# Kernel tuning notes

Measured on AMD Instinct MI355X. Metric: run time of the kernel, lower is better.

Reference implementation:

```python
import jax, jax.numpy as jnp
import numpy as np

NUM_EMBEDDINGS = 2048
BATCH_SIZE = 8
SEQ_LEN = 512
SPATIAL_DIM = 1024
EMBED_DIM = BATCH_SIZE * SEQ_LEN  # 4096
COMMITMENT_COST = 0.25


def setup_inputs() -> dict:
    key = jax.random.key(0)
    k1, k2 = jax.random.split(key)
    inputs = jax.random.normal(k1, (BATCH_SIZE, SEQ_LEN, SPATIAL_DIM), dtype=jnp.float32)
    # original init: uniform(-1/K, 1/K); scaled normal is an acceptable stand-in scale
    embedding = jax.random.uniform(k2, (NUM_EMBEDDINGS, EMBED_DIM), dtype=jnp.float32,
                                   minval=-1.0 / NUM_EMBEDDINGS, maxval=1.0 / NUM_EMBEDDINGS)
    return {"inputs": inputs, "embedding": embedding}


def reference(inputs, embedding):
    B, L, S = inputs.shape
    K, D = embedding.shape
    sg = jax.lax.stop_gradient
    # [S, D] : one feature vector per spatial feature index
    x = jnp.transpose(inputs, (2, 0, 1)).reshape(S, -1)
    # squared-euclidean distances via expansion (avoids S x K x D intermediate)
    d = (jnp.sum(x * x, axis=1, keepdims=True)
         - 2.0 * jnp.einsum('sd,kd->sk', x, embedding)
         + jnp.sum(embedding * embedding, axis=1)[None, :])  # [S, K]
    idx = jnp.argmin(d, axis=1)                 # [S]
    q = embedding[idx]                          # [S, D] gather == one_hot @ E
    # per-feature losses (mse over the (1, D) feature vector == mean over D)
    e_latent = jnp.mean((sg(q) - x) ** 2, axis=1)
    q_latent = jnp.mean((q - sg(x)) ** 2, axis=1)
    total_loss = jnp.mean(q_latent + COMMITMENT_COST * e_latent)
    # straight-through estimator
    q_ste = x + sg(q - x)
    quantized_output = jnp.transpose(q_ste.reshape(S, B, L), (1, 2, 0))  # [B, L, S]
    # per-feature perplexity: encodings is (1, K) one-hot, avg over dim0 is the row itself
    enc = jax.nn.one_hot(idx, K, dtype=x.dtype)  # [S, K]
    perpl = jnp.exp(-jnp.sum(enc * jnp.log(enc + 1e-10), axis=1))  # [S]
    avg_perplexity = jnp.mean(perpl)
    return (total_loss, quantized_output, avg_perplexity, idx)
```

## Files before the change

kernel.cpp:

```cpp
#include <hip/hip_runtime.h>
#include <hip/hip_bf16.h>
#include <math.h>

#define S_DIM 1024
#define K_DIM 2048
#define D_DIM 4096

#define OUT_Q    1
#define OUT_PERP (1 + D_DIM * S_DIM)
#define OUT_IDX  (2 + D_DIM * S_DIM)

#define MARGIN 6.0e-3f
#define CONF_GAP 4.5e-3f
#define FLT_BIG 3.4028235e38f

#define WS_LOSS   0
#define WS_XX     64
#define WS_EE     4160
#define WS_MINP   77888
#define WS_CNT    143424
#define WS_IDX    208960
#define WS_KCAND  213056
#define WS_SCAND  2310208
#define WS_ESTAGE 4407360
#define WS_XSTAGE 21184576
#define WS_BEST   29573184
#define WS_PAIRS  29581376
#define WS_EEP    30105664ull
#define WS_XXP2   31154240ull
#define WS_NEEDED3 31678528ull

#define FB_LOSS 0
#define FB_XX   4096
#define FB_EE   8192
#define FB_XXP  16384
#define FB_MINV 81920
#define FB_MINI 212992
#define FB_IDX  344064

typedef __attribute__((ext_vector_type(8))) short bf16x8;
typedef __attribute__((ext_vector_type(4))) float f32x4;

__device__ __forceinline__ unsigned short f2bf(float f) {
    __hip_bfloat16 h = __float2bfloat16(f);
    return *reinterpret_cast<unsigned short*>(&h);
}

__device__ __forceinline__ void gload16(const void* g, void* l) {
    __builtin_amdgcn_global_load_lds(
        (const __attribute__((address_space(1))) unsigned int*)(g),
        (__attribute__((address_space(3))) unsigned int*)(l), 16, 0, 0);
}

__global__ __launch_bounds__(256) void k_xx_part(const float* __restrict__ A, float* __restrict__ xxp) {
    const int dc = blockIdx.x;
    const int s = blockIdx.y * 256 + threadIdx.x;
    float acc = 0.f;
    for (int dd = 0; dd < 256; ++dd) {
        const int d = dc * 256 + dd;
        float v = A[(size_t)d * S_DIM + s];
        acc = fmaf(v, v, acc);
    }
    xxp[dc * S_DIM + s] = acc;
}

__global__ __launch_bounds__(256) void k_xx_comb(const float* __restrict__ xxp, float* __restrict__ xx) {
    const int s = blockIdx.x * 256 + threadIdx.x;
    float acc = 0.f;
    for (int dc = 0; dc < 16; ++dc) acc += xxp[dc * S_DIM + s];
    xx[s] = acc;
}

__global__ __launch_bounds__(256) void k_ee(const float* __restrict__ E, float* __restrict__ ee) {
    const int k = blockIdx.x;
    const float4* row = (const float4*)(E + (size_t)k * D_DIM);
    float acc = 0.f;
#pragma unroll
    for (int j = 0; j < 4; ++j) {
        float4 v = row[threadIdx.x + j * 256];
        acc = fmaf(v.x, v.x, acc);
        acc = fmaf(v.y, v.y, acc);
        acc = fmaf(v.z, v.z, acc);
        acc = fmaf(v.w, v.w, acc);
    }
    __shared__ float red[256];
    red[threadIdx.x] = acc;
    __syncthreads();
    for (int off = 128; off > 0; off >>= 1) {
        if (threadIdx.x < off) red[threadIdx.x] += red[threadIdx.x + off];
        __syncthreads();
    }
    if (threadIdx.x == 0) ee[k] = red[0];
}

__global__ __launch_bounds__(256) void k_conv(const float* __restrict__ E, const float* __restrict__ A,
                                              float* __restrict__ AT, char* __restrict__ Estage,
                                              char* __restrict__ Xstage, float* __restrict__ eep,
                                              float* __restrict__ xxp2) {
    __shared__ float ldsT[32][65];
    const int dt = blockIdx.x;
    const int tid = threadIdx.x;
    if (blockIdx.y < 16) {
        const int kt = blockIdx.y;
        char* tile = Estage + (size_t)kt * 1048576 + (size_t)dt * 8192;
#pragma unroll
        for (int i = 0; i < 2; ++i) {
            int idx = i * 256 + tid;
            int row = idx >> 2, dc = idx & 3;
            const float4* src = (const float4*)(E + (size_t)(kt * 128 + row) * D_DIM + dt * 32 + dc * 8);
            float4 v0 = src[0], v1 = src[1];
            float vals[8] = {v0.x, v0.y, v0.z, v0.w, v1.x, v1.y, v1.z, v1.w};
            unsigned int w[4];
#pragma unroll
            for (int q = 0; q < 4; ++q)
                w[q] = (unsigned int)f2bf(vals[2 * q]) | ((unsigned int)f2bf(vals[2 * q + 1]) << 16);
            int c_dst = ((row >> 6) * 4 + ((row >> 4) & 3)) * 64 + dc * 16 + (row & 15);
            *(uint4*)(tile + (size_t)c_dst * 16) = make_uint4(w[0], w[1], w[2], w[3]);
            float p = 0.f;
#pragma unroll
            for (int q = 0; q < 8; ++q) p = fmaf(vals[q], vals[q], p);
            p += __shfl_down(p, 2);
            p += __shfl_down(p, 1);
            if ((tid & 3) == 0) eep[(size_t)dt * K_DIM + kt * 128 + row] = p;
        }
    } else {
        const int st = blockIdx.y - 16;
#pragma unroll
        for (int i = 0; i < 2; ++i) {
            int idx = i * 256 + tid;
            int row_d = idx >> 4, c = idx & 15;
            float4 v = *(const float4*)(A + (size_t)(dt * 32 + row_d) * S_DIM + st * 64 + c * 4);
            ldsT[row_d][c * 4 + 0] = v.x;
            ldsT[row_d][c * 4 + 1] = v.y;
            ldsT[row_d][c * 4 + 2] = v.z;
            ldsT[row_d][c * 4 + 3] = v.w;
        }
        __syncthreads();
        {
            int s_row = tid >> 2, dpart = (tid & 3) * 8;
            float vals[8];
#pragma unroll
            for (int j = 0; j < 8; ++j) vals[j] = ldsT[dpart + j][s_row];
            float* dst = AT + (size_t)(st * 64 + s_row) * D_DIM + dt * 32 + dpart;
            *(float4*)(dst + 0) = make_float4(vals[0], vals[1], vals[2], vals[3]);
            *(float4*)(dst + 4) = make_float4(vals[4], vals[5], vals[6], vals[7]);
            float p = 0.f;
#pragma unroll
            for (int j = 0; j < 8; ++j) p = fmaf(vals[j], vals[j], p);
            p += __shfl_down(p, 2);
            p += __shfl_down(p, 1);
            if ((tid & 3) == 0) xxp2[(size_t)dt * S_DIM + st * 64 + s_row] = p;
        }
        {
            int s_row = tid >> 2, dc = tid & 3;
            float vals[8];
#pragma unroll
            for (int j = 0; j < 8; ++j) vals[j] = ldsT[dc * 8 + j][s_row];
            unsigned int w[4];
#pragma unroll
            for (int q = 0; q < 4; ++q)
                w[q] = (unsigned int)f2bf(vals[2 * q]) | ((unsigned int)f2bf(vals[2 * q + 1]) << 16);
            int gn = ((s_row >> 5) << 1) | ((s_row >> 4) & 1);
            int c_dst = gn * 64 + dc * 16 + (s_row & 15);
            char* tile = Xstage + (size_t)st * 524288 + (size_t)dt * 4096;
            *(uint4*)(tile + (size_t)c_dst * 16) = make_uint4(w[0], w[1], w[2], w[3]);
        }
    }
}

__global__ __launch_bounds__(256) void k_sums(const float* __restrict__ eep, const float* __restrict__ xxp2,
                                              float* __restrict__ ee, float* __restrict__ xx,
                                              unsigned long long* __restrict__ best) {
    const int gid = blockIdx.x * 256 + threadIdx.x;
    if (gid < 1024) best[gid] = 0xFFFFFFFFFFFFFFFFull;
    if (gid < K_DIM) {
        float a = 0.f;
        for (int dt = 0; dt < 128; ++dt) a += eep[(size_t)dt * K_DIM + gid];
        ee[gid] = a;
    } else if (gid < K_DIM + S_DIM) {
        const int s = gid - K_DIM;
        float a = 0.f;
        for (int dt = 0; dt < 128; ++dt) a += xxp2[(size_t)dt * S_DIM + s];
        xx[s] = a;
    }
}

__global__ __launch_bounds__(1024) void k_gemm_score5(const char* __restrict__ Estage, const char* __restrict__ Xstage,
                                                      const float* __restrict__ xx, const float* __restrict__ ee,
                                                      float* __restrict__ minp, int* __restrict__ cnt,
                                                      int* __restrict__ kcand, float* __restrict__ scand) {
    __shared__ short lds[4 * 3 * 6144];
    __shared__ float minw[2][64];
    __shared__ float minb[64];
    __shared__ int cntl[64];

    const int linear = blockIdx.y * 16 + blockIdx.x;
    const int xcd = linear & 7, ii = linear >> 3;
    const int ktb = (xcd >> 1) * 4 + (ii >> 3);
    const int st  = (xcd & 1) * 8 + (ii & 7);

    const int tid = threadIdx.x;
    const int h = tid >> 8;
    const int tidh = tid & 255;
    const int wid2 = tidh >> 6;
    const int wm = wid2 >> 1;
    const int wn = wid2 & 1;
    const int lane = tid & 63;
    const int lr = lane & 15;
    const int lh = lane >> 4;

    const char* Eb = Estage + (size_t)ktb * 1048576;
    const char* Xb = Xstage + (size_t)st * 524288;
    short* myl = lds + h * 18432;

    f32x4 acc[4][2];
#pragma unroll
    for (int f = 0; f < 4; ++f)
#pragma unroll
        for (int g = 0; g < 2; ++g) acc[f][g] = (f32x4){0.f, 0.f, 0.f, 0.f};

#define STG(t, sl) { \
    const char* eb_ = Eb + (size_t)(h * 32 + (t)) * 8192; \
    char* d_ = (char*)myl + (sl) * 12288; \
    gload16(eb_ + tidh * 16, d_ + tidh * 16); \
    gload16(eb_ + 4096 + tidh * 16, d_ + 4096 + tidh * 16); \
    gload16(Xb + (size_t)(h * 32 + (t)) * 4096 + tidh * 16, d_ + 8192 + tidh * 16); }

#define CMP(sl) { \
    const short* s_ = myl + (sl) * 6144; \
    bf16x8 af[4], bx[2]; \
    _Pragma("unroll") \
    for (int f = 0; f < 4; ++f) af[f] = *(const bf16x8*)(s_ + (wm * 4 + f) * 512 + lane * 8); \
    _Pragma("unroll") \
    for (int g = 0; g < 2; ++g) bx[g] = *(const bf16x8*)(s_ + 4096 + (wn * 2 + g) * 512 + lane * 8); \
    _Pragma("unroll") \
    for (int f = 0; f < 4; ++f) { \
        _Pragma("unroll") \
        for (int g = 0; g < 2; ++g) \
            acc[f][g] = __builtin_amdgcn_mfma_f32_16x16x32_bf16(af[f], bx[g], acc[f][g], 0, 0, 0); \
    } }

#define WB(nstr) asm volatile("s_waitcnt vmcnt(" nstr ")\n\ts_barrier" ::: "memory")
#define BAR asm volatile("s_barrier" ::: "memory")

    STG(0, 0) STG(1, 1)

    for (int bb = 0; bb < 30; bb += 3) {
        STG(bb + 2, 2) WB("6"); CMP(0) BAR;
        STG(bb + 3, 0) WB("6"); CMP(1) BAR;
        STG(bb + 4, 1) WB("6"); CMP(2) BAR;
    }
    WB("3"); CMP(0) BAR;
    WB("0"); CMP(1)
    __syncthreads();

#undef STG
#undef CMP
#undef WB
#undef BAR

    f32x4* red4 = (f32x4*)lds;
    if (h != 0) {
#pragma unroll
        for (int f = 0; f < 4; ++f)
#pragma unroll
            for (int g = 0; g < 2; ++g)
                red4[(size_t)(h - 1) * 2048 + (f * 2 + g) * 256 + tidh] = acc[f][g];
    }
    __syncthreads();
    if (h == 0) {
#pragma unroll
        for (int q = 1; q < 4; ++q)
#pragma unroll
            for (int f = 0; f < 4; ++f)
#pragma unroll
                for (int g = 0; g < 2; ++g)
                    acc[f][g] += red4[(size_t)(q - 1) * 2048 + (f * 2 + g) * 256 + tidh];
    }

    float xs[2], ek[4][4];
#pragma unroll
    for (int g = 0; g < 2; ++g) xs[g] = xx[st * 64 + wn * 32 + g * 16 + lr];
#pragma unroll
    for (int f = 0; f < 4; ++f)
#pragma unroll
        for (int r = 0; r < 4; ++r) ek[f][r] = ee[ktb * 128 + wm * 64 + f * 16 + lh * 4 + r];

    float mg[2] = {FLT_BIG, FLT_BIG};
#pragma unroll
    for (int f = 0; f < 4; ++f)
#pragma unroll
        for (int g = 0; g < 2; ++g)
#pragma unroll
            for (int r = 0; r < 4; ++r) {
                float sc = (xs[g] - 2.0f * acc[f][g][r]) + ek[f][r];
                mg[g] = fminf(mg[g], sc);
            }
#pragma unroll
    for (int g = 0; g < 2; ++g) {
        mg[g] = fminf(mg[g], __shfl_xor(mg[g], 16));
        mg[g] = fminf(mg[g], __shfl_xor(mg[g], 32));
    }
    if (h == 0 && lane < 16) {
        minw[wm][wn * 32 + lane] = mg[0];
        minw[wm][wn * 32 + 16 + lane] = mg[1];
    }
    __syncthreads();
    if (tid < 64) {
        float mb = fminf(minw[0][tid], minw[1][tid]);
        minb[tid] = mb;
        minp[ktb * S_DIM + st * 64 + tid] = mb;
        cntl[tid] = 0;
    }
    __syncthreads();
    if (h == 0) {
#pragma unroll
        for (int f = 0; f < 4; ++f)
#pragma unroll
            for (int g = 0; g < 2; ++g)
#pragma unroll
                for (int r = 0; r < 4; ++r) {
                    float sc = (xs[g] - 2.0f * acc[f][g][r]) + ek[f][r];
                    int sl = wn * 32 + g * 16 + lr;
                    if (sc <= minb[sl] + MARGIN) {
                        int slot = atomicAdd(&cntl[sl], 1);
                        if (slot < 32) {
                            int si = ktb * S_DIM + st * 64 + sl;
                            kcand[si * 32 + slot] = ktb * 128 + wm * 64 + f * 16 + lh * 4 + r;
                            scand[si * 32 + slot] = sc;
                        }
                    }
                }
    }
    __syncthreads();
    if (tid < 64) cnt[ktb * S_DIM + st * 64 + tid] = min(cntl[tid], 32);
}

__global__ __launch_bounds__(64) void k_select_gate(const float* __restrict__ minp, const int* __restrict__ cnt,
                                                    const int* __restrict__ kcand, const float* __restrict__ scand,
                                                    int* __restrict__ idx, float* __restrict__ out,
                                                    int* __restrict__ npairs, int2* __restrict__ pairs) {
    __shared__ int   lcand[64];
    __shared__ float lsc[64];
    __shared__ int   lcount;
    const int s = blockIdx.x;
    const int lane = threadIdx.x;
    if (lane == 0) lcount = 0;

    float mv = (lane < 16) ? minp[lane * S_DIM + s] : FLT_BIG;
#pragma unroll
    for (int off = 1; off < 64; off <<= 1) mv = fminf(mv, __shfl_xor(mv, off));
    const float m_a = mv;

    int myc = (lane < 16) ? cnt[lane * S_DIM + s] : 0;
    float gsc[16]; int gkc[16]; int gcs[16];
#pragma unroll
    for (int kt = 0; kt < 16; ++kt) {
        int c = __shfl(myc, kt);
        gcs[kt] = c;
        gsc[kt] = FLT_BIG; gkc[kt] = 0;
        if (lane < c) {
            gsc[kt] = scand[(kt * S_DIM + s) * 32 + lane];
            gkc[kt] = kcand[(kt * S_DIM + s) * 32 + lane];
        }
    }
#pragma unroll
    for (int kt = 0; kt < 16; ++kt) {
        if (lane < gcs[kt] && gsc[kt] <= m_a + MARGIN) {
            int slot = atomicAdd(&lcount, 1);
            if (slot < 64) { lcand[slot] = gkc[kt]; lsc[slot] = gsc[kt]; }
        }
    }
    __syncthreads();
    const int n = min(lcount, 64);

    float bv = (lane < n) ? lsc[lane] : FLT_BIG;
    int   bk = (lane < n) ? lcand[lane] : 0x7fffffff;
#pragma unroll
    for (int off = 1; off < 64; off <<= 1) {
        float ov = __shfl_xor(bv, off); int ok = __shfl_xor(bk, off);
        if (ov < bv || (ov == bv && ok < bk)) { bv = ov; bk = ok; }
    }
    float sv = (lane < n && lcand[lane] != bk) ? lsc[lane] : FLT_BIG;
#pragma unroll
    for (int off = 1; off < 64; off <<= 1) sv = fminf(sv, __shfl_xor(sv, off));

    if (n == 1 || sv - bv > CONF_GAP) {
        if (lane == 0) { idx[s] = bk; out[OUT_IDX + s] = (float)bk; }
        return;
    }

    bool em = (lane < n) && (lsc[lane] <= bv + CONF_GAP);
    unsigned long long m = __ballot(em);
    int cnt2 = __popcll(m);
    int base = 0;
    if (lane == 0) base = atomicAdd(npairs, cnt2);
    base = __shfl(base, 0);
    int off2 = (int)__popcll(m & ((1ull << lane) - 1ull));
    if (em) pairs[base + off2] = make_int2(s, lcand[lane]);
}

__global__ __launch_bounds__(64) void k_pair_chain(const float* __restrict__ AT, const float* __restrict__ E,
                                                   const float* __restrict__ xx, const float* __restrict__ ee,
                                                   const int* __restrict__ npairs, const int2* __restrict__ pairs,
                                                   unsigned long long* __restrict__ best) {
    const int np = min(*npairs, 65536);
    const int lane = threadIdx.x;
    for (int p = blockIdx.x; p < np; p += gridDim.x) {
        int2 pr = pairs[p];
        const float4* er4 = (const float4*)(E + (size_t)pr.y * D_DIM) + lane * 16;
        const float4* xr4 = (const float4*)(AT + (size_t)pr.x * D_DIM) + lane * 16;
        float4 er[16], xr[16];
#pragma unroll
        for (int i = 0; i < 16; ++i) { er[i] = er4[i]; xr[i] = xr4[i]; }

        float c = 0.f;
        for (int seg = 0; seg < 64; ++seg) {
            float cin = __shfl(c, (seg + 63) & 63);
            if (lane == seg) {
                float a = (seg == 0) ? 0.f : cin;
#pragma unroll
                for (int i = 0; i < 16; ++i) {
                    a = fmaf(er[i].x, xr[i].x, a);
                    a = fmaf(er[i].y, xr[i].y, a);
                    a = fmaf(er[i].z, xr[i].z, a);
                    a = fmaf(er[i].w, xr[i].w, a);
                }
                c = a;
            }
        }
        float dot = __shfl(c, 63);
        if (lane == 0) {
            float u = xx[pr.x] - 2.0f * dot;
            float sc = u + ee[pr.y];
            unsigned long long pk = ((unsigned long long)__float_as_uint(sc) << 32) | (unsigned int)pr.y;
            atomicMin(&best[pr.x], pk);
        }
    }
}

__global__ __launch_bounds__(256) void k_gemm_argmin(const float* __restrict__ A, const float* __restrict__ E,
                                                     const float* __restrict__ xx, const float* __restrict__ ee,
                                                     float* __restrict__ minv, int* __restrict__ mini) {
    __shared__ float Et[32][64];
    __shared__ float At[32][64];
    __shared__ float rv[16][64];
    __shared__ int   ri[16][64];
    const int kt = blockIdx.x, st = blockIdx.y;
    const int k0 = kt * 64, s0 = st * 64;
    const int tid = threadIdx.x;
    const int tcol = tid & 15, trow = tid >> 4;
    float acc[4][4] = {{0.f,0.f,0.f,0.f},{0.f,0.f,0.f,0.f},{0.f,0.f,0.f,0.f},{0.f,0.f,0.f,0.f}};
    for (int dt = 0; dt < D_DIM / 32; ++dt) {
        const int d0 = dt * 32;
        __syncthreads();
#pragma unroll
        for (int it = 0; it < 2; ++it) {
            int f = tid + it * 256;
            int kk = f >> 3, dd4 = f & 7;
            float4 v = *(const float4*)(E + (size_t)(k0 + kk) * D_DIM + d0 + dd4 * 4);
            Et[dd4 * 4 + 0][kk] = v.x; Et[dd4 * 4 + 1][kk] = v.y;
            Et[dd4 * 4 + 2][kk] = v.z; Et[dd4 * 4 + 3][kk] = v.w;
        }
#pragma unroll
        for (int it = 0; it < 2; ++it) {
            int f = tid + it * 256;
            int ss4 = f & 15, dd = f >> 4;
            float4 v = *(const float4*)(A + (size_t)(d0 + dd) * S_DIM + s0 + ss4 * 4);
            *(float4*)&At[dd][ss4 * 4] = v;
        }
        __syncthreads();
#pragma unroll 8
        for (int dd = 0; dd < 32; ++dd) {
            float4 a4 = *(const float4*)&At[dd][tcol * 4];
            float4 e4 = *(const float4*)&Et[dd][trow * 4];
            float a[4] = {a4.x, a4.y, a4.z, a4.w};
            float e[4] = {e4.x, e4.y, e4.z, e4.w};
#pragma unroll
            for (int i = 0; i < 4; ++i)
#pragma unroll
                for (int j = 0; j < 4; ++j) acc[i][j] = fmaf(e[i], a[j], acc[i][j]);
        }
    }
    float xs[4], ek[4];
#pragma unroll
    for (int j = 0; j < 4; ++j) xs[j] = xx[s0 + tcol * 4 + j];
#pragma unroll
    for (int i = 0; i < 4; ++i) ek[i] = ee[k0 + trow * 4 + i];
#pragma unroll
    for (int j = 0; j < 4; ++j) {
        float bv = FLT_BIG; int bk = 0x7fffffff;
#pragma unroll
        for (int i = 0; i < 4; ++i) {
            float xe = acc[i][j];
            float u = xs[j] - 2.0f * xe;
            float sc = u + ek[i];
            int k = k0 + trow * 4 + i;
            if (sc < bv) { bv = sc; bk = k; }
        }
        rv[trow][tcol * 4 + j] = bv;
        ri[trow][tcol * 4 + j] = bk;
    }
    __syncthreads();
    if (tid < 64) {
        float bv = rv[0][tid]; int bk = ri[0][tid];
#pragma unroll
        for (int r = 1; r < 16; ++r) {
            float v = rv[r][tid]; int k2 = ri[r][tid];
            if (v < bv || (v == bv && k2 < bk)) { bv = v; bk = k2; }
        }
        minv[kt * S_DIM + s0 + tid] = bv;
        mini[kt * S_DIM + s0 + tid] = bk;
    }
}

__global__ __launch_bounds__(256) void k_argmin_final(const float* __restrict__ minv, const int* __restrict__ mini,
                                                      int* __restrict__ idx, float* __restrict__ out) {
    const int s = blockIdx.x * 256 + threadIdx.x;
    float bv = minv[s];
    int bk = mini[s];
    for (int kt = 1; kt < 32; ++kt) {
        float v = minv[kt * S_DIM + s];
        int k2 = mini[kt * S_DIM + s];
        if (v < bv || (v == bv && k2 < bk)) { bv = v; bk = k2; }
    }
    idx[s] = bk;
    out[OUT_IDX + s] = (float)bk;
}

__global__ __launch_bounds__(256) void k_output_loss2(const float* __restrict__ A, const float* __restrict__ E,
                                                      const int* __restrict__ idx,
                                                      const unsigned long long* __restrict__ best,
                                                      float* __restrict__ out, float* __restrict__ loss) {
    __shared__ float qt[64][65];
    __shared__ int sidx[64];
    __shared__ float red[256];
    const int st = blockIdx.x, dtb = blockIdx.y;
    const int s0 = st * 64, d0 = dtb * 64;
    const int tid = threadIdx.x;
    if (tid < 64) {
        const int s = s0 + tid;
        unsigned long long b = best[s];
        int k;
        if (b != 0xFFFFFFFFFFFFFFFFull) {
            k = (int)(b & 0xFFFFFFFFu);
            if (dtb == 0) out[OUT_IDX + s] = (float)k;
        } else {
            k = idx[s];
        }
        sidx[tid] = k;
    }
    __syncthreads();
#pragma unroll
    for (int it = 0; it < 4; ++it) {
        int f = tid + it * 256;
        int si = f >> 4, c4 = f & 15;
        float4 v = *(const float4*)(E + (size_t)sidx[si] * D_DIM + d0 + c4 * 4);
        qt[si][c4 * 4 + 0] = v.x; qt[si][c4 * 4 + 1] = v.y;
        qt[si][c4 * 4 + 2] = v.z; qt[si][c4 * 4 + 3] = v.w;
    }
    __syncthreads();
    const int ss = tid & 63;
    const int dg = tid >> 6;
    float lsum = 0.f;
#pragma unroll
    for (int i = 0; i < 16; ++i) {
        const int dd = dg * 16 + i;
        const int d = d0 + dd;
        float x = A[(size_t)d * S_DIM + s0 + ss];
        float q = qt[ss][dd];
        float diff = q - x;
        float val = x + diff;
        out[OUT_Q + (size_t)d * S_DIM + s0 + ss] = val;
        lsum = fmaf(diff, diff, lsum);
    }
    red[tid] = lsum;
    __syncthreads();
    for (int off = 128; off > 0; off >>= 1) {
        if (tid < off) red[tid] += red[tid + off];
        __syncthreads();
    }
    if (tid == 0) atomicAdd(loss, red[0]);
}

__global__ __launch_bounds__(256) void k_output_loss(const float* __restrict__ A, const float* __restrict__ E,
                                                     const int* __restrict__ idx, float* __restrict__ out,
                                                     float* __restrict__ loss) {
    __shared__ float qt[64][65];
    __shared__ int sidx[64];
    __shared__ float red[256];
    const int st = blockIdx.x, dtb = blockIdx.y;
    const int s0 = st * 64, d0 = dtb * 64;
    const int tid = threadIdx.x;
    if (tid < 64) sidx[tid] = idx[s0 + tid];
    __syncthreads();
#pragma unroll
    for (int it = 0; it < 4; ++it) {
        int f = tid + it * 256;
        int si = f >> 4, c4 = f & 15;
        float4 v = *(const float4*)(E + (size_t)sidx[si] * D_DIM + d0 + c4 * 4);
        qt[si][c4 * 4 + 0] = v.x; qt[si][c4 * 4 + 1] = v.y;
        qt[si][c4 * 4 + 2] = v.z; qt[si][c4 * 4 + 3] = v.w;
    }
    __syncthreads();
    const int ss = tid & 63;
    const int dg = tid >> 6;
    float lsum = 0.f;
#pragma unroll
    for (int i = 0; i < 16; ++i) {
        const int dd = dg * 16 + i;
        const int d = d0 + dd;
        float x = A[(size_t)d * S_DIM + s0 + ss];
        float q = qt[ss][dd];
        float diff = q - x;
        float val = x + diff;
        out[OUT_Q + (size_t)d * S_DIM + s0 + ss] = val;
        lsum = fmaf(diff, diff, lsum);
    }
    red[tid] = lsum;
    __syncthreads();
    for (int off = 128; off > 0; off >>= 1) {
        if (tid < off) red[tid] += red[tid + off];
        __syncthreads();
    }
    if (tid == 0) atomicAdd(loss, red[0]);
}

__global__ void k_scalars(const float* __restrict__ loss, float* __restrict__ out) {
    out[0] = 1.25f * loss[0] * (1.0f / (float)(S_DIM * D_DIM));
    out[OUT_PERP] = 1.0f;
}

extern "C" void kernel_launch(void* const* d_in, const int* in_sizes, int n_in,
                              void* d_out, int out_size, void* d_ws, size_t ws_size,
                              hipStream_t stream) {
    const float* A = (const float*)d_in[0];
    const float* E = (const float*)d_in[1];
    float* out = (float*)d_out;
    char* ws = (char*)d_ws;

    if (ws_size >= WS_NEEDED3) {
        float* w_loss = (float*)(ws + WS_LOSS);
        int*   w_np   = (int*)(ws + 16);
        float* w_xx   = (float*)(ws + WS_XX);
        float* w_ee   = (float*)(ws + WS_EE);
        float* w_minp = (float*)(ws + WS_MINP);
        int*   w_cnt  = (int*)(ws + WS_CNT);
        int*   w_idx  = (int*)(ws + WS_IDX);
        int*   w_kc   = (int*)(ws + WS_KCAND);
        float* w_sc   = (float*)(ws + WS_SCAND);
        char*  w_es   = ws + WS_ESTAGE;
        char*  w_xs   = ws + WS_XSTAGE;
        unsigned long long* w_best = (unsigned long long*)(ws + WS_BEST);
        int2*  w_pairs = (int2*)(ws + WS_PAIRS);
        float* w_eep  = (float*)(ws + WS_EEP);
        float* w_xxp2 = (float*)(ws + WS_XXP2);
        float* AT     = out + OUT_Q;

        hipMemsetAsync(ws, 0, 64, stream);
        k_conv<<<dim3(128, 32), 256, 0, stream>>>(E, A, AT, w_es, w_xs, w_eep, w_xxp2);
        k_sums<<<dim3(12), 256, 0, stream>>>(w_eep, w_xxp2, w_ee, w_xx, w_best);
        k_gemm_score5<<<dim3(16, 16), 1024, 0, stream>>>(w_es, w_xs, w_xx, w_ee, w_minp, w_cnt, w_kc, w_sc);
        k_select_gate<<<dim3(S_DIM), 64, 0, stream>>>(w_minp, w_cnt, w_kc, w_sc, w_idx, out, w_np, w_pairs);
        k_pair_chain<<<dim3(2048), 64, 0, stream>>>(AT, E, w_xx, w_ee, w_np, w_pairs, w_best);
        k_output_loss2<<<dim3(16, 64), 256, 0, stream>>>(A, E, w_idx, w_best, out, w_loss);
        k_scalars<<<1, 1, 0, stream>>>(w_loss, out);
    } else {
        float* w_loss = (float*)(ws + FB_LOSS);
        float* w_xx   = (float*)(ws + FB_XX);
        float* w_ee   = (float*)(ws + FB_EE);
        float* w_xxp  = (float*)(ws + FB_XXP);
        float* w_minv = (float*)(ws + FB_MINV);
        int*   w_mini = (int*)(ws + FB_MINI);
        int*   w_idx  = (int*)(ws + FB_IDX);

        hipMemsetAsync(ws, 0, 256, stream);
        k_xx_part<<<dim3(16, 4), 256, 0, stream>>>(A, w_xxp);
        k_ee<<<dim3(K_DIM), 256, 0, stream>>>(E, w_ee);
        k_xx_comb<<<dim3(4), 256, 0, stream>>>(w_xxp, w_xx);
        k_gemm_argmin<<<dim3(32, 16), 256, 0, stream>>>(A, E, w_xx, w_ee, w_minv, w_mini);
        k_argmin_final<<<dim3(4), 256, 0, stream>>>(w_minv, w_mini, w_idx, out);
        k_output_loss<<<dim3(16, 64), 256, 0, stream>>>(A, E, w_idx, out, w_loss);
        k_scalars<<<1, 1, 0, stream>>>(w_loss, out);
    }
}
```

Baseline: 112.6 us.

## Fold norm sums into GEMM epilogue and finalize scalars in last loss block

Removes the separate k_sums and k_scalars launches. The GEMM kernel now reduces the partial codebook and input norms for its own tile into shared memory, and selected blocks write them to global memory for later kernels. The reset of the best-pair array moves into the select kernel. The final loss and perplexity scalars are written by the last-arriving block of the loss kernel, found through an atomic arrival counter. This trades two small kernel launches for redundant norm reductions in every GEMM block and a fence-plus-atomic epilogue.

```diff
diff --git a/kernel.cpp b/kernel.cpp
--- a/kernel.cpp
+++ b/kernel.cpp
@@ -168,27 +168,11 @@
     }
 }
 
-__global__ __launch_bounds__(256) void k_sums(const float* __restrict__ eep, const float* __restrict__ xxp2,
-                                              float* __restrict__ ee, float* __restrict__ xx,
-                                              unsigned long long* __restrict__ best) {
-    const int gid = blockIdx.x * 256 + threadIdx.x;
-    if (gid < 1024) best[gid] = 0xFFFFFFFFFFFFFFFFull;
-    if (gid < K_DIM) {
-        float a = 0.f;
-        for (int dt = 0; dt < 128; ++dt) a += eep[(size_t)dt * K_DIM + gid];
-        ee[gid] = a;
-    } else if (gid < K_DIM + S_DIM) {
-        const int s = gid - K_DIM;
-        float a = 0.f;
-        for (int dt = 0; dt < 128; ++dt) a += xxp2[(size_t)dt * S_DIM + s];
-        xx[s] = a;
-    }
-}
-
-__global__ __launch_bounds__(1024) void k_gemm_score5(const char* __restrict__ Estage, const char* __restrict__ Xstage,
-                                                      const float* __restrict__ xx, const float* __restrict__ ee,
-                                                      float* __restrict__ minp, int* __restrict__ cnt,
-                                                      int* __restrict__ kcand, float* __restrict__ scand) {
+__global__ __launch_bounds__(1024) void k_gemm_score5b(const char* __restrict__ Estage, const char* __restrict__ Xstage,
+                                                       float* __restrict__ xx, float* __restrict__ ee,
+                                                       const float* __restrict__ eep, const float* __restrict__ xxp2,
+                                                       float* __restrict__ minp, int* __restrict__ cnt,
+                                                       int* __restrict__ kcand, float* __restrict__ scand) {
     __shared__ short lds[4 * 3 * 6144];
     __shared__ float minw[2][64];
     __shared__ float minb[64];
@@ -260,6 +244,7 @@
 #undef BAR
 
     f32x4* red4 = (f32x4*)lds;
+    float* sl = (float*)((char*)lds + 98304);
     if (h != 0) {
 #pragma unroll
         for (int f = 0; f < 4; ++f)
@@ -267,6 +252,18 @@
             for (int g = 0; g < 2; ++g)
                 red4[(size_t)(h - 1) * 2048 + (f * 2 + g) * 256 + tidh] = acc[f][g];
     }
+    if (h == 3) {
+        if (tidh < 128) {
+            float a = 0.f;
+            for (int dt = 0; dt < 128; ++dt) a += eep[(size_t)dt * K_DIM + ktb * 128 + tidh];
+            sl[tidh] = a;
+        } else if (tidh < 192) {
+            const int s = tidh - 128;
+            float a = 0.f;
+            for (int dt = 0; dt < 128; ++dt) a += xxp2[(size_t)dt * S_DIM + st * 64 + s];
+            sl[128 + s] = a;
+        }
+    }
     __syncthreads();
     if (h == 0) {
 #pragma unroll
@@ -277,14 +274,18 @@
                 for (int g = 0; g < 2; ++g)
                     acc[f][g] += red4[(size_t)(q - 1) * 2048 + (f * 2 + g) * 256 + tidh];
     }
+    if (h == 2) {
+        if (st == 0 && tidh < 128) ee[ktb * 128 + tidh] = sl[tidh];
+        if (ktb == 0 && tidh >= 128 && tidh < 192) xx[st * 64 + (tidh - 128)] = sl[tidh];
+    }
 
     float xs[2], ek[4][4];
 #pragma unroll
-    for (int g = 0; g < 2; ++g) xs[g] = xx[st * 64 + wn * 32 + g * 16 + lr];
+    for (int g = 0; g < 2; ++g) xs[g] = sl[128 + wn * 32 + g * 16 + lr];
 #pragma unroll
     for (int f = 0; f < 4; ++f)
 #pragma unroll
-        for (int r = 0; r < 4; ++r) ek[f][r] = ee[ktb * 128 + wm * 64 + f * 16 + lh * 4 + r];
+        for (int r = 0; r < 4; ++r) ek[f][r] = sl[wm * 64 + f * 16 + lh * 4 + r];
 
     float mg[2] = {FLT_BIG, FLT_BIG};
 #pragma unroll
@@ -321,11 +322,11 @@
 #pragma unroll
                 for (int r = 0; r < 4; ++r) {
                     float sc = (xs[g] - 2.0f * acc[f][g][r]) + ek[f][r];
-                    int sl = wn * 32 + g * 16 + lr;
-                    if (sc <= minb[sl] + MARGIN) {
-                        int slot = atomicAdd(&cntl[sl], 1);
+                    int sl2 = wn * 32 + g * 16 + lr;
+                    if (sc <= minb[sl2] + MARGIN) {
+                        int slot = atomicAdd(&cntl[sl2], 1);
                         if (slot < 32) {
-                            int si = ktb * S_DIM + st * 64 + sl;
+                            int si = ktb * S_DIM + st * 64 + sl2;
                             kcand[si * 32 + slot] = ktb * 128 + wm * 64 + f * 16 + lh * 4 + r;
                             scand[si * 32 + slot] = sc;
                         }
@@ -339,13 +340,14 @@
 __global__ __launch_bounds__(64) void k_select_gate(const float* __restrict__ minp, const int* __restrict__ cnt,
                                                     const int* __restrict__ kcand, const float* __restrict__ scand,
                                                     int* __restrict__ idx, float* __restrict__ out,
-                                                    int* __restrict__ npairs, int2* __restrict__ pairs) {
+                                                    int* __restrict__ npairs, int2* __restrict__ pairs,
+                                                    unsigned long long* __restrict__ best) {
     __shared__ int   lcand[64];
     __shared__ float lsc[64];
     __shared__ int   lcount;
     const int s = blockIdx.x;
     const int lane = threadIdx.x;
-    if (lane == 0) lcount = 0;
+    if (lane == 0) { lcount = 0; best[s] = 0xFFFFFFFFFFFFFFFFull; }
 
     float mv = (lane < 16) ? minp[lane * S_DIM + s] : FLT_BIG;
 #pragma unroll
@@ -531,7 +533,8 @@
 __global__ __launch_bounds__(256) void k_output_loss2(const float* __restrict__ A, const float* __restrict__ E,
                                                       const int* __restrict__ idx,
                                                       const unsigned long long* __restrict__ best,
-                                                      float* __restrict__ out, float* __restrict__ loss) {
+                                                      float* __restrict__ out, float* __restrict__ loss,
+                                                      int* __restrict__ arrive) {
     __shared__ float qt[64][65];
     __shared__ int sidx[64];
     __shared__ float red[256];
@@ -580,7 +583,16 @@
         if (tid < off) red[tid] += red[tid + off];
         __syncthreads();
     }
-    if (tid == 0) atomicAdd(loss, red[0]);
+    if (tid == 0) {
+        atomicAdd(loss, red[0]);
+        __threadfence();
+        int t = atomicAdd(arrive, 1);
+        if (t == 1023) {
+            float L = atomicAdd(loss, 0.0f);
+            out[0] = 1.25f * L * (1.0f / (float)(S_DIM * D_DIM));
+            out[OUT_PERP] = 1.0f;
+        }
+    }
 }
 
 __global__ __launch_bounds__(256) void k_output_loss(const float* __restrict__ A, const float* __restrict__ E,
@@ -642,6 +654,7 @@
     if (ws_size >= WS_NEEDED3) {
         float* w_loss = (float*)(ws + WS_LOSS);
         int*   w_np   = (int*)(ws + 16);
+        int*   w_arr  = (int*)(ws + 32);
         float* w_xx   = (float*)(ws + WS_XX);
         float* w_ee   = (float*)(ws + WS_EE);
         float* w_minp = (float*)(ws + WS_MINP);
@@ -659,12 +672,11 @@
 
         hipMemsetAsync(ws, 0, 64, stream);
         k_conv<<<dim3(128, 32), 256, 0, stream>>>(E, A, AT, w_es, w_xs, w_eep, w_xxp2);
-        k_sums<<<dim3(12), 256, 0, stream>>>(w_eep, w_xxp2, w_ee, w_xx, w_best);
-        k_gemm_score5<<<dim3(16, 16), 1024, 0, stream>>>(w_es, w_xs, w_xx, w_ee, w_minp, w_cnt, w_kc, w_sc);
-        k_select_gate<<<dim3(S_DIM), 64, 0, stream>>>(w_minp, w_cnt, w_kc, w_sc, w_idx, out, w_np, w_pairs);
+        k_gemm_score5b<<<dim3(16, 16), 1024, 0, stream>>>(w_es, w_xs, w_xx, w_ee, w_eep, w_xxp2,
+                                                          w_minp, w_cnt, w_kc, w_sc);
+        k_select_gate<<<dim3(S_DIM), 64, 0, stream>>>(w_minp, w_cnt, w_kc, w_sc, w_idx, out, w_np, w_pairs, w_best);
         k_pair_chain<<<dim3(2048), 64, 0, stream>>>(AT, E, w_xx, w_ee, w_np, w_pairs, w_best);
-        k_output_loss2<<<dim3(16, 64), 256, 0, stream>>>(A, E, w_idx, w_best, out, w_loss);
-        k_scalars<<<1, 1, 0, stream>>>(w_loss, out);
+        k_output_loss2<<<dim3(16, 64), 256, 0, stream>>>(A, E, w_idx, w_best, out, w_loss, w_arr);
     } else {
         float* w_loss = (float*)(ws + FB_LOSS);
         float* w_xx   = (float*)(ws + FB_XX);
```

Result: slower. 132.4 us (+17.6%).
